# Kernel optimization log

Hardware: AMD Instinct MI355X
Metric: run time of the kernel (lower is better)

Reference implementation:

```python
import jax, jax.numpy as jnp
import numpy as np

N = 100_000      # nodes
E = 1_600_000    # edges (avg degree 16)
IN_DIM = 165
HIDDEN = 64
OUT_DIM = 2


def setup_inputs() -> dict:
    key = jax.random.key(0)
    ks = jax.random.split(key, 10)
    x = jax.random.normal(ks[0], (N, IN_DIM), dtype=jnp.float32)
    edge_index = jax.random.randint(ks[1], (2, E), 0, N, dtype=jnp.int32)
    def lin(k, fan_in, fan_out):
        lim = 1.0 / np.sqrt(fan_in)
        return jax.random.uniform(k, (fan_in, fan_out), jnp.float32, -lim, lim)
    # SAGEConv: lin_l (neighbor path, with bias), lin_r (root path, no bias)
    W1l = lin(ks[2], IN_DIM, HIDDEN); b1 = jnp.zeros((HIDDEN,), jnp.float32)
    W1r = lin(ks[3], IN_DIM, HIDDEN)
    W2l = lin(ks[4], HIDDEN, HIDDEN); b2 = jnp.zeros((HIDDEN,), jnp.float32)
    W2r = lin(ks[5], HIDDEN, HIDDEN)
    Wc = lin(ks[6], HIDDEN, OUT_DIM)
    bc = jax.random.uniform(ks[7], (OUT_DIM,), jnp.float32, -0.1, 0.1)
    return {"x": x, "edge_index": edge_index, "W1l": W1l, "b1": b1, "W1r": W1r,
            "W2l": W2l, "b2": b2, "W2r": W2r, "Wc": Wc, "bc": bc}


def _sage_conv(h, src, dst, Wl, bl, Wr):
    # mean-aggregate source features at destination nodes, then two linears
    msg = h[src]                                              # [E, D] gather
    agg = jax.ops.segment_sum(msg, dst, num_segments=N)       # [N, D] scatter-add
    cnt = jax.ops.segment_sum(jnp.ones((src.shape[0], 1), h.dtype), dst,
                              num_segments=N)                 # [N, 1] in-degree
    mean = agg / jnp.maximum(cnt, 1.0)
    return mean @ Wl + bl + h @ Wr


def reference(x, edge_index, W1l, b1, W1r, W2l, b2, W2r, Wc, bc):
    src, dst = edge_index[0], edge_index[1]
    h = jax.nn.relu(_sage_conv(x, src, dst, W1l, b1, W1r))
    # dropout is a no-op at inference (training=False)
    h = jax.nn.relu(_sage_conv(h, src, dst, W2l, b2, W2r))
    return h @ Wc + bc
```

## Files before the change

### kernel.cpp

```cpp
#include <hip/hip_runtime.h>
#include <hip/hip_fp16.h>
#include <cstdint>

#define NN 100000
#define NE 1600000
#define INDIM 165
#define HID 64
#define KP1 192
#define KP2 64

constexpr int BSH = 7;
constexpr int BNODES = 128;
constexpr int NBUK = (NN + BNODES - 1) / BNODES;
constexpr int SC_CHUNK = 8192;
constexpr int BCAP = 2816;

typedef _Float16 f16x8 __attribute__((ext_vector_type(8)));
typedef _Float16 h2 __attribute__((ext_vector_type(2)));
typedef float f32x4 __attribute__((ext_vector_type(4)));

__device__ __forceinline__ void gload16(const float* g, float* l) {
    __builtin_amdgcn_global_load_lds(
        (const __attribute__((address_space(1))) uint32_t*)g,
        (__attribute__((address_space(3))) uint32_t*)l, 16, 0, 0);
}


__global__ __launch_bounds__(256) void k_bscan(const int* __restrict__ bcnt,
                                               int* __restrict__ bbase) {
    __shared__ int wsum[4];
    const int tid = threadIdx.x, lane = tid & 63, wid = tid >> 6;
    int v[4];
    int tsum = 0;
#pragma unroll
    for (int i = 0; i < 4; ++i) {
        int idx = tid * 4 + i;
        v[i] = (idx < NBUK) ? bcnt[idx] : 0;
        tsum += v[i];
    }
    int x = tsum;
#pragma unroll
    for (int off = 1; off < 64; off <<= 1) {
        int y = __shfl_up(x, off, 64);
        if (lane >= off) x += y;
    }
    if (lane == 63) wsum[wid] = x;
    __syncthreads();
    int woff = 0;
#pragma unroll
    for (int w = 0; w < 4; ++w)
        if (w < wid) woff += wsum[w];
    int run = woff + x - tsum;
#pragma unroll
    for (int i = 0; i < 4; ++i) {
        int idx = tid * 4 + i;
        if (idx < NBUK) bbase[idx] = run;
        run += v[i];
    }
    if (tid == 255) bbase[NBUK] = woff + x;
}


__global__ __launch_bounds__(256) void k_scatter(const int* __restrict__ src,
                                                 const int* __restrict__ dst,
                                                 int* __restrict__ bcnt,
                                                 unsigned* __restrict__ Eb, int ne) {
    __shared__ int hist[NBUK];
    __shared__ int base[NBUK];
    const int tid = threadIdx.x;
    const int cs = blockIdx.x * SC_CHUNK;
    for (int b = tid; b < NBUK; b += 256) hist[b] = 0;
    __syncthreads();
    unsigned pack[SC_CHUNK / 256];
#pragma unroll 8
    for (int i = 0; i < SC_CHUNK / 256; ++i) {
        int e = cs + i * 256 + tid;
        if (e < ne) {
            int b = dst[e] >> BSH;
            int r = atomicAdd(&hist[b], 1);
            pack[i] = (unsigned)((b << 13) | r);
        } else {
            pack[i] = 0xFFFFFFFFu;
        }
    }
    __syncthreads();
    for (int b = tid; b < NBUK; b += 256) {
        int c = hist[b];
        base[b] = c ? atomicAdd(&bcnt[b], c) : 0;
    }
    __syncthreads();
#pragma unroll 8
    for (int i = 0; i < SC_CHUNK / 256; ++i) {
        if (pack[i] != 0xFFFFFFFFu) {
            int e = cs + i * 256 + tid;
            int b = pack[i] >> 13, r = pack[i] & 8191;
            int pos = base[b] + r;
            if (pos < BCAP)
                Eb[(size_t)b * BCAP + pos] =
                    (unsigned)src[e] | ((unsigned)(dst[e] & (BNODES - 1)) << 17);
        }
    }
}


__global__ __launch_bounds__(256) void k_csrb(const unsigned* __restrict__ Eb,
                                              const int* __restrict__ bbase,
                                              int* __restrict__ rowptr,
                                              int* __restrict__ col, int n) {
    __shared__ int cnt[BNODES];
    __shared__ int pref[BNODES];
    const int tid = threadIdx.x;
    const int gb = bbase[blockIdx.x];
    const int m = bbase[blockIdx.x + 1] - gb;
    const unsigned* eb = Eb + (size_t)blockIdx.x * BCAP;
    for (int i = tid; i < BNODES; i += 256) cnt[i] = 0;
    __syncthreads();
    for (int e = tid; e < m; e += 256)
        atomicAdd(&cnt[eb[e] >> 17], 1);
    __syncthreads();
    if (tid < 64) {
        int c0 = cnt[tid * 2], c1 = cnt[tid * 2 + 1];
        int s = c0 + c1;
        int x = s;
#pragma unroll
        for (int off = 1; off < 64; off <<= 1) {
            int y = __shfl_up(x, off, 64);
            if (tid >= off) x += y;
        }
        int ex = x - s;
        pref[tid * 2] = ex;
        pref[tid * 2 + 1] = ex + c0;
    }
    __syncthreads();
    const int nodeBase = blockIdx.x * BNODES;
    for (int i = tid; i < BNODES; i += 256) {
        int gn = nodeBase + i;
        if (gn < n) rowptr[gn] = gb + pref[i];
        cnt[i] = 0;
    }
    __syncthreads();
    for (int e = tid; e < m; e += 256) {
        unsigned v = eb[e];
        int d = (int)(v >> 17);
        int r = atomicAdd(&cnt[d], 1);
        col[gb + pref[d] + r] = (int)(v & 0x1FFFFu);
    }
    if (blockIdx.x == 0 && tid == 0) rowptr[n] = bbase[NBUK];
}


__global__ __launch_bounds__(256) void k_wcvt(const float* __restrict__ W1l,
                                              const float* __restrict__ W1r,
                                              const float* __restrict__ W2l,
                                              const float* __restrict__ W2r,
                                              _Float16* __restrict__ Wt1,
                                              _Float16* __restrict__ Wt2) {
    int o = blockIdx.x * 256 + threadIdx.x;
    if (o < 128 * KP1) {
        int c = o / KP1, k = o - c * KP1;
        float v = 0.f;
        if (k < INDIM) v = (c < HID) ? W1l[k * HID + c] : W1r[k * HID + (c - HID)];
        Wt1[o] = (_Float16)v;
    } else if (o < 128 * KP1 + 128 * KP2) {
        int p = o - 128 * KP1;
        int c = p / KP2, k = p - c * KP2;
        float v = (c < HID) ? W2l[k * HID + c] : W2r[k * HID + (c - HID)];
        Wt2[p] = (_Float16)v;
    }
}


__global__ __launch_bounds__(256) void k_lin1(const float* __restrict__ X,
                                              const _Float16* __restrict__ Wt,
                                              _Float16* __restrict__ Y,
                                              _Float16* __restrict__ Rh, int n) {
    constexpr int ROWD = INDIM;
    constexpr int LDSZ = 64 * 168;
    __shared__ float Xs[LDSZ];
    const int tid = threadIdx.x;
    const int lane = tid & 63;
    const int wi = tid >> 6;
    const int jn = lane & 15;
    const int kq = lane >> 4;
    const int r0 = blockIdx.x * 64;
    const int vr = (n - r0 < 64) ? (n - r0) : 64;
    const int cnt = vr * ROWD;
    const int nFull = cnt >> 8;
    const float* __restrict__ P = X + (size_t)r0 * ROWD;

    for (int i = cnt + tid; i < cnt + 192 && i < LDSZ; i += 256) Xs[i] = 0.f;

    for (int i = wi; i < nFull; i += 4)
        gload16(P + i * 256 + lane * 4, Xs + i * 256);
    for (int i = (nFull << 8) + tid; i < cnt; i += 256) Xs[i] = P[i];
    __syncthreads();

    const _Float16* wp = Wt + (size_t)jn * KP1 + kq * 8;
    const float* xrow = &Xs[(wi * 16 + jn) * ROWD + kq * 8];

    f32x4 acc[8];
#pragma unroll
    for (int t = 0; t < 8; ++t) acc[t] = (f32x4){0.f, 0.f, 0.f, 0.f};

#pragma unroll
    for (int c = 0; c < 6; ++c) {
        f16x8 xb;
#pragma unroll
        for (int j = 0; j < 8; ++j) xb[j] = (_Float16)xrow[c * 32 + j];
#pragma unroll
        for (int t = 0; t < 8; ++t) {
            const f16x8 wa = *(const f16x8*)(wp + t * (16 * KP1) + c * 32);
            acc[t] = __builtin_amdgcn_mfma_f32_16x16x32_f16(wa, xb, acc[t], 0, 0, 0);
        }
    }

    const int gn0 = r0 + wi * 16 + jn;
    if (gn0 < n) {
#pragma unroll
        for (int t = 0; t < 8; ++t) {
            const int cb = (t & 3) * 16 + kq * 4;
            union { _Float16 h[4]; uint2 u; } u;
#pragma unroll
            for (int r = 0; r < 4; ++r) u.h[r] = (_Float16)acc[t][r];
            _Float16* dstp = (t < 4) ? (Y + (size_t)gn0 * HID + cb)
                                     : (Rh + (size_t)gn0 * HID + cb);
            *(uint2*)dstp = u.u;
        }
    }
}


template <int KPAD>
__global__ __launch_bounds__(256, 4) void k_linear(const _Float16* __restrict__ Xh,
                                                   const _Float16* __restrict__ Wt,
                                                   _Float16* __restrict__ Y,
                                                   _Float16* __restrict__ Rh, int n) {
    const int tid = threadIdx.x;
    const int lane = tid & 63;
    const int w = tid >> 6;
    const int jn = lane & 15;
    const int kq = lane >> 4;
    const int gn0 = blockIdx.x * 64 + w * 16 + jn;
    const int gn = (gn0 < n) ? gn0 : (n - 1);

    const _Float16* xp = Xh + (size_t)gn * KPAD + kq * 8;
    const _Float16* wp = Wt + (size_t)jn * KPAD + kq * 8;

    f16x8 xf[KPAD / 32];
#pragma unroll
    for (int c = 0; c < KPAD / 32; ++c)
        xf[c] = *(const f16x8*)(xp + c * 32);

    f32x4 acc[8];
#pragma unroll
    for (int t = 0; t < 8; ++t) acc[t] = (f32x4){0.f, 0.f, 0.f, 0.f};

#pragma unroll
    for (int c = 0; c < KPAD / 32; ++c) {
#pragma unroll
        for (int t = 0; t < 8; ++t) {
            const f16x8 wa = *(const f16x8*)(wp + t * (16 * KPAD) + c * 32);
            acc[t] = __builtin_amdgcn_mfma_f32_16x16x32_f16(wa, xf[c], acc[t], 0, 0, 0);
        }
    }

    if (gn0 < n) {
#pragma unroll
        for (int t = 0; t < 8; ++t) {
            const int cb = (t & 3) * 16 + kq * 4;
            union { _Float16 h[4]; uint2 u; } u;
#pragma unroll
            for (int r = 0; r < 4; ++r) u.h[r] = (_Float16)acc[t][r];
            _Float16* dstp = (t < 4) ? (Y + (size_t)gn * HID + cb)
                                     : (Rh + (size_t)gn * HID + cb);
            *(uint2*)dstp = u.u;
        }
    }
}


__device__ __forceinline__ void acc2(float& ax, float& ay, h2 v) {
    ax += (float)v[0];
    ay += (float)v[1];
}

template <bool CLS>
__global__ __launch_bounds__(256) void k_agg(const _Float16* __restrict__ Y,
                                             const _Float16* __restrict__ Rm,
                                             const float* __restrict__ bias,
                                             const int* __restrict__ rowptr,
                                             const int* __restrict__ col,
                                             _Float16* __restrict__ H,
                                             const float* __restrict__ Wc,
                                             const float* __restrict__ bc,
                                             float* __restrict__ out, int n) {
    const int lane = threadIdx.x & 63;
    const int node = blockIdx.x * 4 + (threadIdx.x >> 6);
    if (node >= n) return;
    const int half_ = lane >> 5;
    const unsigned fp = (unsigned)(lane & 31);
    const h2* __restrict__ Y2 = (const h2*)Y;
    const int s = rowptr[node], e = rowptr[node + 1];
    float ax0 = 0.f, ay0 = 0.f, ax1 = 0.f, ay1 = 0.f;
    int i = s + half_;
    for (; i + 14 < e; i += 16) {
        int c[8];
#pragma unroll
        for (int j = 0; j < 8; ++j) c[j] = col[i + 2 * j];
        h2 y[8];
#pragma unroll
        for (int j = 0; j < 8; ++j) y[j] = Y2[(unsigned)c[j] * 32u + fp];
#pragma unroll
        for (int j = 0; j < 8; j += 2) {
            acc2(ax0, ay0, y[j]);
            acc2(ax1, ay1, y[j + 1]);
        }
    }
    for (; i + 6 < e; i += 8) {
        int c[4];
#pragma unroll
        for (int j = 0; j < 4; ++j) c[j] = col[i + 2 * j];
        h2 y[4];
#pragma unroll
        for (int j = 0; j < 4; ++j) y[j] = Y2[(unsigned)c[j] * 32u + fp];
        acc2(ax0, ay0, y[0]);
        acc2(ax1, ay1, y[1]);
        acc2(ax0, ay0, y[2]);
        acc2(ax1, ay1, y[3]);
    }
    for (; i < e; i += 2)
        acc2(ax0, ay0, Y2[(unsigned)col[i] * 32u + fp]);
    float ax = ax0 + ax1, ay = ay0 + ay1;
    ax += __shfl_xor(ax, 32, 64);
    ay += __shfl_xor(ay, 32, 64);
    const float vx = __shfl(ax, lane >> 1, 64);
    const float vy = __shfl(ay, lane >> 1, 64);
    const float acc = (lane & 1) ? vy : vx;
    const int deg = e - s;
    float h = acc / (float)(deg > 1 ? deg : 1) + bias[lane] +
              (float)Rm[(size_t)node * HID + lane];
    h = fmaxf(h, 0.f);
    if (!CLS) {
        H[(size_t)node * HID + lane] = (_Float16)h;
    } else {
        float p0 = h * Wc[lane * 2 + 0];
        float p1 = h * Wc[lane * 2 + 1];
#pragma unroll
        for (int off = 32; off > 0; off >>= 1) {
            p0 += __shfl_xor(p0, off, 64);
            p1 += __shfl_xor(p1, off, 64);
        }
        if (lane == 0) {
            out[(size_t)node * 2 + 0] = p0 + bc[0];
            out[(size_t)node * 2 + 1] = p1 + bc[1];
        }
    }
}


extern "C" void kernel_launch(void* const* d_in, const int* in_sizes, int n_in,
                              void* d_out, int out_size, void* d_ws, size_t ws_size,
                              hipStream_t stream) {
    const float* x   = (const float*)d_in[0];
    const int*   ei  = (const int*)d_in[1];
    const float* W1l = (const float*)d_in[2];
    const float* b1  = (const float*)d_in[3];
    const float* W1r = (const float*)d_in[4];
    const float* W2l = (const float*)d_in[5];
    const float* b2  = (const float*)d_in[6];
    const float* W2r = (const float*)d_in[7];
    const float* Wc  = (const float*)d_in[8];
    const float* bc  = (const float*)d_in[9];
    float* out = (float*)d_out;
    const int* src = ei;
    const int* dst = ei + NE;

    char* base = (char*)d_ws;
    size_t off = 0;
    auto alloc = [&](size_t bytes) {
        void* p = base + off;
        off = (off + bytes + 255) & ~(size_t)255;
        return p;
    };
    int*      bcnt    = (int*)alloc((size_t)NBUK * 4);
    int*      bbase   = (int*)alloc((size_t)(NBUK + 1) * 4);
    int*      rowptr  = (int*)alloc((size_t)(NN + 1) * 4);
    int*      col     = (int*)alloc((size_t)NE * 4);
    _Float16* Y       = (_Float16*)alloc((size_t)NN * HID * 2 + 256);
    _Float16* Rh      = (_Float16*)alloc((size_t)NN * HID * 2);
    _Float16* Hh      = (_Float16*)alloc((size_t)NN * HID * 2);
    _Float16* Wt1     = (_Float16*)alloc((size_t)128 * KP1 * 2);
    _Float16* Wt2     = (_Float16*)alloc((size_t)128 * KP2 * 2);
    unsigned* Eb      = (unsigned*)Y;

    const int sb = (NE + SC_CHUNK - 1) / SC_CHUNK;
    const int wb = (128 * KP1 + 128 * KP2 + 255) / 256;

    hipMemsetAsync(bcnt, 0, (size_t)NBUK * 4, stream);
    k_scatter<<<sb, 256, 0, stream>>>(src, dst, bcnt, Eb, NE);
    k_bscan<<<1, 256, 0, stream>>>(bcnt, bbase);
    k_csrb<<<NBUK, 256, 0, stream>>>(Eb, bbase, rowptr, col, NN);
    k_wcvt<<<wb, 256, 0, stream>>>(W1l, W1r, W2l, W2r, Wt1, Wt2);

    k_lin1<<<(NN + 63) / 64, 256, 0, stream>>>(x, Wt1, Y, Rh, NN);
    k_agg<false><<<(NN + 3) / 4, 256, 0, stream>>>(Y, Rh, b1, rowptr, col, Hh,
                                                   nullptr, nullptr, nullptr, NN);
    k_linear<KP2><<<(NN + 63) / 64, 256, 0, stream>>>(Hh, Wt2, Y, Rh, NN);
    k_agg<true><<<(NN + 3) / 4, 256, 0, stream>>>(Y, Rh, b2, rowptr, col, nullptr,
                                                  Wc, bc, out, NN);
}
```

Measured before the change: 324.7 us.

## Fuse layer-1 aggregation with layer-2 linear and merge weight conversion into scan

```diff
diff --git a/kernel.cpp b/kernel.cpp
--- a/kernel.cpp
+++ b/kernel.cpp
@@ -27,7 +27,28 @@
 
 
 __global__ __launch_bounds__(256) void k_bscan(const int* __restrict__ bcnt,
-                                               int* __restrict__ bbase) {
+                                               int* __restrict__ bbase,
+                                               const float* __restrict__ W1l,
+                                               const float* __restrict__ W1r,
+                                               const float* __restrict__ W2l,
+                                               const float* __restrict__ W2r,
+                                               _Float16* __restrict__ Wt1,
+                                               _Float16* __restrict__ Wt2) {
+    if (blockIdx.x > 0) {
+        int o = (blockIdx.x - 1) * 256 + threadIdx.x;
+        if (o < 128 * KP1) {
+            int c = o / KP1, k = o - c * KP1;
+            float v = 0.f;
+            if (k < INDIM) v = (c < HID) ? W1l[k * HID + c] : W1r[k * HID + (c - HID)];
+            Wt1[o] = (_Float16)v;
+        } else if (o < 128 * KP1 + 128 * KP2) {
+            int p = o - 128 * KP1;
+            int c = p / KP2, k = p - c * KP2;
+            float v = (c < HID) ? W2l[k * HID + c] : W2r[k * HID + (c - HID)];
+            Wt2[p] = (_Float16)v;
+        }
+        return;
+    }
     __shared__ int wsum[4];
     const int tid = threadIdx.x, lane = tid & 63, wid = tid >> 6;
     int v[4];
@@ -149,34 +170,12 @@
 }
 
 
-__global__ __launch_bounds__(256) void k_wcvt(const float* __restrict__ W1l,
-                                              const float* __restrict__ W1r,
-                                              const float* __restrict__ W2l,
-                                              const float* __restrict__ W2r,
-                                              _Float16* __restrict__ Wt1,
-                                              _Float16* __restrict__ Wt2) {
-    int o = blockIdx.x * 256 + threadIdx.x;
-    if (o < 128 * KP1) {
-        int c = o / KP1, k = o - c * KP1;
-        float v = 0.f;
-        if (k < INDIM) v = (c < HID) ? W1l[k * HID + c] : W1r[k * HID + (c - HID)];
-        Wt1[o] = (_Float16)v;
-    } else if (o < 128 * KP1 + 128 * KP2) {
-        int p = o - 128 * KP1;
-        int c = p / KP2, k = p - c * KP2;
-        float v = (c < HID) ? W2l[k * HID + c] : W2r[k * HID + (c - HID)];
-        Wt2[p] = (_Float16)v;
-    }
-}
-
-
 __global__ __launch_bounds__(256) void k_lin1(const float* __restrict__ X,
                                               const _Float16* __restrict__ Wt,
                                               _Float16* __restrict__ Y,
                                               _Float16* __restrict__ Rh, int n) {
-    constexpr int ROWD = INDIM;
-    constexpr int LDSZ = 64 * 168;
-    __shared__ float Xs[LDSZ];
+    constexpr int WROWD = 16 * INDIM;
+    __shared__ float Xs[4 * WROWD];
     const int tid = threadIdx.x;
     const int lane = tid & 63;
     const int wi = tid >> 6;
@@ -184,19 +183,24 @@
     const int kq = lane >> 4;
     const int r0 = blockIdx.x * 64;
     const int vr = (n - r0 < 64) ? (n - r0) : 64;
-    const int cnt = vr * ROWD;
-    const int nFull = cnt >> 8;
-    const float* __restrict__ P = X + (size_t)r0 * ROWD;
-
-    for (int i = cnt + tid; i < cnt + 192 && i < LDSZ; i += 256) Xs[i] = 0.f;
-
-    for (int i = wi; i < nFull; i += 4)
-        gload16(P + i * 256 + lane * 4, Xs + i * 256);
-    for (int i = (nFull << 8) + tid; i < cnt; i += 256) Xs[i] = P[i];
-    __syncthreads();
-
+    const int cnt = vr * INDIM;
+    const float* __restrict__ P = X + (size_t)r0 * INDIM;
+
+    const int myS = wi * WROWD;
+    int d = cnt - myS;
+    if (d > WROWD) d = WROWD;
+    if (d > 0) {
+        const int nd = d >> 8;
+        for (int i = 0; i < nd; ++i)
+            gload16(P + myS + i * 256 + lane * 4, Xs + myS + i * 256);
+        for (int i = myS + (nd << 8) + lane; i < myS + d; i += 64)
+            Xs[i] = P[i];
+        asm volatile("s_waitcnt vmcnt(0)" ::: "memory");
+        __builtin_amdgcn_sched_barrier(0);
+    }
+
+    const float* xrow = &Xs[(wi * 16 + jn) * INDIM + kq * 8];
     const _Float16* wp = Wt + (size_t)jn * KP1 + kq * 8;
-    const float* xrow = &Xs[(wi * 16 + jn) * ROWD + kq * 8];
 
     f32x4 acc[8];
 #pragma unroll
@@ -205,8 +209,14 @@
 #pragma unroll
     for (int c = 0; c < 6; ++c) {
         f16x8 xb;
-#pragma unroll
-        for (int j = 0; j < 8; ++j) xb[j] = (_Float16)xrow[c * 32 + j];
+        if (c < 5) {
+#pragma unroll
+            for (int j = 0; j < 8; ++j) xb[j] = (_Float16)xrow[c * 32 + j];
+        } else {
+#pragma unroll
+            for (int j = 0; j < 8; ++j)
+                xb[j] = (kq == 0 && j < 5) ? (_Float16)xrow[160 + j] : (_Float16)0.f;
+        }
 #pragma unroll
         for (int t = 0; t < 8; ++t) {
             const f16x8 wa = *(const f16x8*)(wp + t * (16 * KP1) + c * 32);
@@ -230,40 +240,95 @@
 }
 
 
-template <int KPAD>
-__global__ __launch_bounds__(256, 4) void k_linear(const _Float16* __restrict__ Xh,
+__device__ __forceinline__ void acc2(float& ax, float& ay, h2 v) {
+    ax += (float)v[0];
+    ay += (float)v[1];
+}
+
+__global__ __launch_bounds__(256, 4) void k_agglin(const _Float16* __restrict__ Yin,
+                                                   const _Float16* __restrict__ Rin,
+                                                   const float* __restrict__ bias,
+                                                   const int* __restrict__ rowptr,
+                                                   const int* __restrict__ col,
                                                    const _Float16* __restrict__ Wt,
-                                                   _Float16* __restrict__ Y,
-                                                   _Float16* __restrict__ Rh, int n) {
+                                                   _Float16* __restrict__ Yout,
+                                                   _Float16* __restrict__ Rout,
+                                                   int n) {
+    __shared__ _Float16 Hs[64][72];
     const int tid = threadIdx.x;
     const int lane = tid & 63;
-    const int w = tid >> 6;
+    const int wi = tid >> 6;
+    const int nodeBase = blockIdx.x * 64;
+    const int half_ = lane >> 5;
+    const unsigned fp = (unsigned)(lane & 31);
+    const h2* __restrict__ Y2c = (const h2*)Yin;
+
+    for (int t = 0; t < 16; ++t) {
+        const int ln = wi * 16 + t;
+        const int node = nodeBase + ln;
+        if (node >= n) continue;
+        const int s = rowptr[node], e = rowptr[node + 1];
+        float ax0 = 0.f, ay0 = 0.f, ax1 = 0.f, ay1 = 0.f;
+        int i = s + half_;
+        for (; i + 14 < e; i += 16) {
+            int c[8];
+#pragma unroll
+            for (int j = 0; j < 8; ++j) c[j] = col[i + 2 * j];
+            h2 y[8];
+#pragma unroll
+            for (int j = 0; j < 8; ++j) y[j] = Y2c[(unsigned)c[j] * 32u + fp];
+#pragma unroll
+            for (int j = 0; j < 8; j += 2) {
+                acc2(ax0, ay0, y[j]);
+                acc2(ax1, ay1, y[j + 1]);
+            }
+        }
+        for (; i + 6 < e; i += 8) {
+            int c[4];
+#pragma unroll
+            for (int j = 0; j < 4; ++j) c[j] = col[i + 2 * j];
+            h2 y[4];
+#pragma unroll
+            for (int j = 0; j < 4; ++j) y[j] = Y2c[(unsigned)c[j] * 32u + fp];
+            acc2(ax0, ay0, y[0]);
+            acc2(ax1, ay1, y[1]);
+            acc2(ax0, ay0, y[2]);
+            acc2(ax1, ay1, y[3]);
+        }
+        for (; i < e; i += 2)
+            acc2(ax0, ay0, Y2c[(unsigned)col[i] * 32u + fp]);
+        float ax = ax0 + ax1, ay = ay0 + ay1;
+        ax += __shfl_xor(ax, 32, 64);
+        ay += __shfl_xor(ay, 32, 64);
+        const float vx = __shfl(ax, lane >> 1, 64);
+        const float vy = __shfl(ay, lane >> 1, 64);
+        const float acc = (lane & 1) ? vy : vx;
+        const int deg = e - s;
+        float h = acc / (float)(deg > 1 ? deg : 1) + bias[lane] +
+                  (float)Rin[(size_t)node * HID + lane];
+        Hs[ln][lane] = (_Float16)fmaxf(h, 0.f);
+    }
+
     const int jn = lane & 15;
     const int kq = lane >> 4;
-    const int gn0 = blockIdx.x * 64 + w * 16 + jn;
-    const int gn = (gn0 < n) ? gn0 : (n - 1);
-
-    const _Float16* xp = Xh + (size_t)gn * KPAD + kq * 8;
-    const _Float16* wp = Wt + (size_t)jn * KPAD + kq * 8;
-
-    f16x8 xf[KPAD / 32];
-#pragma unroll
-    for (int c = 0; c < KPAD / 32; ++c)
-        xf[c] = *(const f16x8*)(xp + c * 32);
+    const _Float16* wp = Wt + (size_t)jn * KP2 + kq * 8;
+    const _Float16* xp = &Hs[wi * 16 + jn][0];
 
     f32x4 acc[8];
 #pragma unroll
     for (int t = 0; t < 8; ++t) acc[t] = (f32x4){0.f, 0.f, 0.f, 0.f};
 
 #pragma unroll
-    for (int c = 0; c < KPAD / 32; ++c) {
+    for (int c = 0; c < 2; ++c) {
+        const f16x8 xb = *(const f16x8*)(xp + c * 32 + kq * 8);
 #pragma unroll
         for (int t = 0; t < 8; ++t) {
-            const f16x8 wa = *(const f16x8*)(wp + t * (16 * KPAD) + c * 32);
-            acc[t] = __builtin_amdgcn_mfma_f32_16x16x32_f16(wa, xf[c], acc[t], 0, 0, 0);
-        }
-    }
-
+            const f16x8 wa = *(const f16x8*)(wp + t * (16 * KP2) + c * 32);
+            acc[t] = __builtin_amdgcn_mfma_f32_16x16x32_f16(wa, xb, acc[t], 0, 0, 0);
+        }
+    }
+
+    const int gn0 = nodeBase + wi * 16 + jn;
     if (gn0 < n) {
 #pragma unroll
         for (int t = 0; t < 8; ++t) {
@@ -271,29 +336,22 @@
             union { _Float16 h[4]; uint2 u; } u;
 #pragma unroll
             for (int r = 0; r < 4; ++r) u.h[r] = (_Float16)acc[t][r];
-            _Float16* dstp = (t < 4) ? (Y + (size_t)gn * HID + cb)
-                                     : (Rh + (size_t)gn * HID + cb);
+            _Float16* dstp = (t < 4) ? (Yout + (size_t)gn0 * HID + cb)
+                                     : (Rout + (size_t)gn0 * HID + cb);
             *(uint2*)dstp = u.u;
         }
     }
 }
 
 
-__device__ __forceinline__ void acc2(float& ax, float& ay, h2 v) {
-    ax += (float)v[0];
-    ay += (float)v[1];
-}
-
-template <bool CLS>
-__global__ __launch_bounds__(256) void k_agg(const _Float16* __restrict__ Y,
-                                             const _Float16* __restrict__ Rm,
-                                             const float* __restrict__ bias,
-                                             const int* __restrict__ rowptr,
-                                             const int* __restrict__ col,
-                                             _Float16* __restrict__ H,
-                                             const float* __restrict__ Wc,
-                                             const float* __restrict__ bc,
-                                             float* __restrict__ out, int n) {
+__global__ __launch_bounds__(256) void k_aggc(const _Float16* __restrict__ Y,
+                                              const _Float16* __restrict__ Rm,
+                                              const float* __restrict__ bias,
+                                              const int* __restrict__ rowptr,
+                                              const int* __restrict__ col,
+                                              const float* __restrict__ Wc,
+                                              const float* __restrict__ bc,
+                                              float* __restrict__ out, int n) {
     const int lane = threadIdx.x & 63;
     const int node = blockIdx.x * 4 + (threadIdx.x >> 6);
     if (node >= n) return;
@@ -340,20 +398,16 @@
     float h = acc / (float)(deg > 1 ? deg : 1) + bias[lane] +
               (float)Rm[(size_t)node * HID + lane];
     h = fmaxf(h, 0.f);
-    if (!CLS) {
-        H[(size_t)node * HID + lane] = (_Float16)h;
-    } else {
-        float p0 = h * Wc[lane * 2 + 0];
-        float p1 = h * Wc[lane * 2 + 1];
-#pragma unroll
-        for (int off = 32; off > 0; off >>= 1) {
-            p0 += __shfl_xor(p0, off, 64);
-            p1 += __shfl_xor(p1, off, 64);
-        }
-        if (lane == 0) {
-            out[(size_t)node * 2 + 0] = p0 + bc[0];
-            out[(size_t)node * 2 + 1] = p1 + bc[1];
-        }
+    float p0 = h * Wc[lane * 2 + 0];
+    float p1 = h * Wc[lane * 2 + 1];
+#pragma unroll
+    for (int off = 32; off > 0; off >>= 1) {
+        p0 += __shfl_xor(p0, off, 64);
+        p1 += __shfl_xor(p1, off, 64);
+    }
+    if (lane == 0) {
+        out[(size_t)node * 2 + 0] = p0 + bc[0];
+        out[(size_t)node * 2 + 1] = p1 + bc[1];
     }
 }
 
@@ -388,24 +442,23 @@
     int*      col     = (int*)alloc((size_t)NE * 4);
     _Float16* Y       = (_Float16*)alloc((size_t)NN * HID * 2 + 256);
     _Float16* Rh      = (_Float16*)alloc((size_t)NN * HID * 2);
-    _Float16* Hh      = (_Float16*)alloc((size_t)NN * HID * 2);
+    _Float16* Y2      = (_Float16*)alloc((size_t)NN * HID * 2);
+    _Float16* Rh2     = (_Float16*)alloc((size_t)NN * HID * 2);
     _Float16* Wt1     = (_Float16*)alloc((size_t)128 * KP1 * 2);
     _Float16* Wt2     = (_Float16*)alloc((size_t)128 * KP2 * 2);
     unsigned* Eb      = (unsigned*)Y;
 
     const int sb = (NE + SC_CHUNK - 1) / SC_CHUNK;
-    const int wb = (128 * KP1 + 128 * KP2 + 255) / 256;
+    const int wb = 1 + (128 * KP1 + 128 * KP2 + 255) / 256;
 
     hipMemsetAsync(bcnt, 0, (size_t)NBUK * 4, stream);
     k_scatter<<<sb, 256, 0, stream>>>(src, dst, bcnt, Eb, NE);
-    k_bscan<<<1, 256, 0, stream>>>(bcnt, bbase);
+    k_bscan<<<wb, 256, 0, stream>>>(bcnt, bbase, W1l, W1r, W2l, W2r, Wt1, Wt2);
     k_csrb<<<NBUK, 256, 0, stream>>>(Eb, bbase, rowptr, col, NN);
-    k_wcvt<<<wb, 256, 0, stream>>>(W1l, W1r, W2l, W2r, Wt1, Wt2);
 
     k_lin1<<<(NN + 63) / 64, 256, 0, stream>>>(x, Wt1, Y, Rh, NN);
-    k_agg<false><<<(NN + 3) / 4, 256, 0, stream>>>(Y, Rh, b1, rowptr, col, Hh,
-                                                   nullptr, nullptr, nullptr, NN);
-    k_linear<KP2><<<(NN + 63) / 64, 256, 0, stream>>>(Hh, Wt2, Y, Rh, NN);
-    k_agg<true><<<(NN + 3) / 4, 256, 0, stream>>>(Y, Rh, b2, rowptr, col, nullptr,
-                                                  Wc, bc, out, NN);
-}
+    k_agglin<<<(NN + 63) / 64, 256, 0, stream>>>(Y, Rh, b1, rowptr, col, Wt2,
+                                                 Y2, Rh2, NN);
+    k_aggc<<<(NN + 3) / 4, 256, 0, stream>>>(Y2, Rh2, b2, rowptr, col,
+                                             Wc, bc, out, NN);
+}
```

Result: slower. 346.5 us (+6.7%).
